# Kernel tuning notes

Measured on AMD Instinct MI355X. Metric: run time of the kernel, lower is better.

Reference implementation:

```python
import jax, jax.numpy as jnp
import numpy as np

N_NODES = 100000
N_EDGES = 625000
D = 128
DEPTH = 2
BN_EPS = 1e-5


def setup_inputs() -> dict:
    key = jax.random.key(0)
    ks = jax.random.split(key, 8)
    x = jax.random.normal(ks[0], (N_NODES, D), dtype=jnp.float32)
    edge_index = jax.random.randint(ks[1], (2, N_EDGES), 0, N_NODES, dtype=jnp.int64)
    edge_weight = jax.random.uniform(ks[2], (N_EDGES,), dtype=jnp.float32)
    s = 1.0 / np.sqrt(D)
    W_lin = jax.random.uniform(ks[3], (DEPTH, D, D), jnp.float32, -s, s)
    W_gcn = jax.random.uniform(ks[4], (DEPTH, D, D), jnp.float32, -s, s)
    gamma = jnp.ones((DEPTH, D), jnp.float32)
    beta = jnp.zeros((DEPTH, D), jnp.float32)
    return {"x": x, "edge_index": edge_index, "edge_weight": edge_weight,
            "W_lin": W_lin, "W_gcn": W_gcn, "gamma": gamma, "beta": beta}


def reference(x, edge_index, edge_weight, W_lin, W_gcn, gamma, beta):
    n = x.shape[0]
    row, col = edge_index[0], edge_index[1]  # source, target
    # gcn_norm with add_self_loops=False: deg over targets, symmetric normalization
    deg = jax.ops.segment_sum(edge_weight, col, num_segments=n)
    dinv = jnp.where(deg > 0, jax.lax.rsqrt(deg), 0.0)
    norm = dinv[row] * edge_weight * dinv[col]  # [E]

    for i in range(DEPTH):
        hl = x @ W_lin[i].T                       # parallel linear branch
        hg = x @ W_gcn[i].T                       # GCNConv linear
        msg = norm[:, None] * hg[row]             # [E, D] messages
        hr = jax.ops.segment_sum(msg, col, num_segments=n)
        h = hl + hr
        # BatchNorm1d, training mode (batch statistics, biased variance)
        mu = jnp.mean(h, axis=0)
        var = jnp.mean((h - mu) ** 2, axis=0)
        h = (h - mu) * jax.lax.rsqrt(var + BN_EPS) * gamma[i] + beta[i]
        x = jnp.maximum(h, 0.0) if i != DEPTH - 1 else h
    return x
```

## Files before the change

### kernel.cpp

```cpp
#include <hip/hip_runtime.h>

#define NN 100000
#define NE 625000
#define DD 128
#define CAP 32
#define NREP 8

#define CONVB 12500
#define WPACKB 256
#define FILL2B ((NE / 2 + 255) / 256)
#define GB ((NN + 63) / 64)

typedef __attribute__((ext_vector_type(8))) short bf16x8;
typedef __attribute__((ext_vector_type(4))) float f32x4;

static __device__ __forceinline__ unsigned short f2bf(float f) {
    union { float f; unsigned u; } v; v.f = f;
    unsigned u = v.u + 0x7fffu + ((v.u >> 16) & 1u);
    return (unsigned short)(u >> 16);
}
static __device__ __forceinline__ float bflo(unsigned u) { return __uint_as_float(u << 16); }
static __device__ __forceinline__ float bfhi(unsigned u) { return __uint_as_float(u & 0xffff0000u); }

static __device__ __forceinline__ void foldLDS(const float* __restrict__ stats,
                                               const float* __restrict__ gamma,
                                               const float* __restrict__ beta,
                                               float* sSc, float* sSh, int t) {
    if (t < 128) {
        float sum = 0.f, sq = 0.f;
        #pragma unroll
        for (int rp = 0; rp < NREP; rp++) {
            sum += stats[rp * 256 + t];
            sq  += stats[rp * 256 + 128 + t];
        }
        float mu = sum * (1.0f / NN);
        float var = sq * (1.0f / NN) - mu * mu;
        float is = rsqrtf(var + 1e-5f);
        float sc = is * gamma[t];
        sSc[t] = sc;
        sSh[t] = beta[t] - mu * sc;
    }
}

__global__ __launch_bounds__(256) void k_fill(const int* __restrict__ row,
                                              const int* __restrict__ col,
                                              const float* __restrict__ w,
                                              int* __restrict__ cnt,
                                              int2* __restrict__ ebuf) {
    int id = blockIdx.x * 256 + threadIdx.x;
    if (id < NE / 2) {
        int e = id * 2;
        int2 rr = *(const int2*)&row[e];
        int2 cc = *(const int2*)&col[e];
        float2 ww = *(const float2*)&w[e];
        int p0 = atomicAdd(&cnt[cc.x], 1);
        int p1 = atomicAdd(&cnt[cc.y], 1);
        if (p0 < CAP) {
            int2 v; v.x = rr.x; v.y = __float_as_int(ww.x);
            ebuf[(size_t)cc.x * CAP + p0] = v;
        }
        if (p1 < CAP) {
            int2 v; v.x = rr.y; v.y = __float_as_int(ww.y);
            ebuf[(size_t)cc.y * CAP + p1] = v;
        }
    }
}

__global__ __launch_bounds__(256) void k_conv(const float* __restrict__ x,
                                              unsigned* __restrict__ Xb2,
                                              const float* __restrict__ Wl,
                                              const float* __restrict__ Wg,
                                              unsigned short* __restrict__ wp) {
    int b = blockIdx.x, t = threadIdx.x;
    if (b < WPACKB) {
        int idx = b * 256 + t;
        int l = idx >> 15;
        int rem = idx & 32767;
        int n = rem >> 8;
        int k = rem & 255;
        float v = (k < 128) ? Wl[(size_t)l * DD * DD + n * DD + k]
                            : Wg[(size_t)l * DD * DD + n * DD + (k - 128)];
        int wv = n >> 5;
        int tt = (n >> 4) & 1;
        int i  = n & 15;
        int ss = k >> 5;
        int q  = (k >> 3) & 3;
        int j  = k & 7;
        size_t off = ((size_t)((((l * 4 + wv) * 2 + tt) * 8 + ss)) * 64 + q * 16 + i) * 8 + j;
        wp[off] = f2bf(v);
    } else {
        size_t i = (size_t)(b - WPACKB) * 256 + t;
        size_t base = i * 4;
        float4 v = *(const float4*)&x[base];
        uint2 o;
        o.x = (unsigned)f2bf(v.x) | ((unsigned)f2bf(v.y) << 16);
        o.y = (unsigned)f2bf(v.z) | ((unsigned)f2bf(v.w) << 16);
        *(uint2*)&Xb2[i * 2] = o;
    }
}

__global__ __launch_bounds__(256) void k_dinvb(const int* __restrict__ cnt,
                                               const int2* __restrict__ ebuf,
                                               float* __restrict__ dinv) {
    int t = threadIdx.x;
    int node = blockIdx.x * 32 + (t >> 3);
    int l = t & 7;
    int c = cnt[node]; if (c > CAP) c = CAP;
    float s = 0.f;
    for (int p = l; p < c; p += 8) s += __int_as_float(ebuf[(size_t)node * CAP + p].y);
    s += __shfl_down(s, 4, 8);
    s += __shfl_down(s, 2, 8);
    s += __shfl_down(s, 1, 8);
    if (l == 0) dinv[node] = (s > 0.f) ? rsqrtf(s) : 0.f;
}

template<int LAYER>
__global__ __launch_bounds__(256) void k_gatherP(const int* __restrict__ cnt,
                                                 const int2* __restrict__ ebuf,
                                                 const float* __restrict__ dinv,
                                                 const unsigned* __restrict__ X2,
                                                 const float* __restrict__ stats,
                                                 const float* __restrict__ gamma,
                                                 const float* __restrict__ beta,
                                                 unsigned* __restrict__ P2) {
    __shared__ float sSc[128], sSh[128];
    const int t = threadIdx.x;
    const int wave = t >> 6;
    const int lane = t & 63;
    float scx = 0.f, scy = 0.f, shx = 0.f, shy = 0.f;
    if (LAYER) {
        foldLDS(stats, gamma, beta, sSc, sSh, t);
        __syncthreads();
        scx = sSc[2 * lane]; scy = sSc[2 * lane + 1];
        shx = sSh[2 * lane]; shy = sSh[2 * lane + 1];
    }

    const int node0 = blockIdx.x * 8 + wave * 2;
    const int node1 = node0 + 1;
    int c0 = cnt[node0]; if (c0 > CAP) c0 = CAP;
    int c1 = cnt[node1]; if (c1 > CAP) c1 = CAP;
    const int2* eb0 = ebuf + (size_t)node0 * CAP;
    const int2* eb1 = ebuf + (size_t)node1 * CAP;
    float ax0 = 0.f, ay0 = 0.f, ax1 = 0.f, ay1 = 0.f;

    auto chunk4 = [&](const int2* __restrict__ eb, int p, float& ax, float& ay) {
        int2 e0 = eb[p], e1 = eb[p + 1], e2 = eb[p + 2], e3 = eb[p + 3];
        float w0 = __int_as_float(e0.y) * dinv[e0.x];
        float w1 = __int_as_float(e1.y) * dinv[e1.x];
        float w2 = __int_as_float(e2.y) * dinv[e2.x];
        float w3 = __int_as_float(e3.y) * dinv[e3.x];
        unsigned u0 = X2[(size_t)e0.x * 64 + lane];
        unsigned u1 = X2[(size_t)e1.x * 64 + lane];
        unsigned u2 = X2[(size_t)e2.x * 64 + lane];
        unsigned u3 = X2[(size_t)e3.x * 64 + lane];
        float x0 = bflo(u0), y0 = bfhi(u0);
        float x1 = bflo(u1), y1 = bfhi(u1);
        float x2 = bflo(u2), y2 = bfhi(u2);
        float x3 = bflo(u3), y3 = bfhi(u3);
        if (LAYER) {
            x0 = fmaxf(x0 * scx + shx, 0.f); y0 = fmaxf(y0 * scy + shy, 0.f);
            x1 = fmaxf(x1 * scx + shx, 0.f); y1 = fmaxf(y1 * scy + shy, 0.f);
            x2 = fmaxf(x2 * scx + shx, 0.f); y2 = fmaxf(y2 * scy + shy, 0.f);
            x3 = fmaxf(x3 * scx + shx, 0.f); y3 = fmaxf(y3 * scy + shy, 0.f);
        }
        ax += w0 * x0 + w1 * x1 + w2 * x2 + w3 * x3;
        ay += w0 * y0 + w1 * y1 + w2 * y2 + w3 * y3;
    };
    auto edge1 = [&](const int2* __restrict__ eb, int p, float& ax, float& ay) {
        int2 e0 = eb[p];
        float w0 = __int_as_float(e0.y) * dinv[e0.x];
        unsigned u0 = X2[(size_t)e0.x * 64 + lane];
        float x0 = bflo(u0), y0 = bfhi(u0);
        if (LAYER) {
            x0 = fmaxf(x0 * scx + shx, 0.f); y0 = fmaxf(y0 * scy + shy, 0.f);
        }
        ax += w0 * x0;
        ay += w0 * y0;
    };

    const int mc = (c0 < c1) ? c0 : c1;
    int p = 0;
    for (; p + 3 < mc; p += 4) {
        chunk4(eb0, p, ax0, ay0);
        chunk4(eb1, p, ax1, ay1);
    }
    int p0 = p, p1 = p;
    for (; p0 + 3 < c0; p0 += 4) chunk4(eb0, p0, ax0, ay0);
    for (; p0 < c0; p0++)        edge1(eb0, p0, ax0, ay0);
    for (; p1 + 3 < c1; p1 += 4) chunk4(eb1, p1, ax1, ay1);
    for (; p1 < c1; p1++)        edge1(eb1, p1, ax1, ay1);

    float dn0 = dinv[node0], dn1 = dinv[node1];
    ax0 *= dn0; ay0 *= dn0;
    ax1 *= dn1; ay1 *= dn1;
    P2[(size_t)node0 * 64 + lane] = (unsigned)f2bf(ax0) | ((unsigned)f2bf(ay0) << 16);
    P2[(size_t)node1 * 64 + lane] = (unsigned)f2bf(ax1) | ((unsigned)f2bf(ay1) << 16);
}

template<int LAYER>
__global__ __launch_bounds__(256, 5) void k_gemm_s(const unsigned short* Xin,
                                                   const unsigned short* P,
                                                   const unsigned short* __restrict__ wp,
                                                   const float* __restrict__ statsIn,
                                                   const float* __restrict__ gammaIn,
                                                   const float* __restrict__ betaIn,
                                                   unsigned short* Hout,
                                                   float* __restrict__ statsOut) {
    __shared__ __align__(16) char smem[22528];
    unsigned short* sA = (unsigned short*)smem;
    float* red2 = (float*)(smem + 17408);
    float* sSc = (float*)(smem + 21504);
    float* sSh = (float*)(smem + 22016);

    const int t = threadIdx.x;
    const int wave = t >> 6;
    const int lane = t & 63;
    const int i16 = lane & 15;
    const int quad = lane >> 4;
    const int rowBase = blockIdx.x * 64;

    if (LAYER == 1) {
        foldLDS(statsIn, gammaIn, betaIn, sSc, sSh, t);
        __syncthreads();
    }

    f32x4 acc[4][2] = {{{0.f,0.f,0.f,0.f}}};

    #pragma unroll
    for (int rep = 0; rep < 4; rep++) {
        int lin = rep * 2048 + t * 8;
        int r = lin >> 7, c = lin & 127;
        int rr = rowBase + r; if (rr >= NN) rr = NN - 1;
        uint4 u = *(const uint4*)&Xin[(size_t)rr * DD + c];
        if (LAYER == 1) {
            float4 sc0 = *(const float4*)&sSc[c];
            float4 sc1 = *(const float4*)&sSc[c + 4];
            float4 sh0 = *(const float4*)&sSh[c];
            float4 sh1 = *(const float4*)&sSh[c + 4];
            float v0 = fmaxf(bflo(u.x) * sc0.x + sh0.x, 0.f);
            float v1 = fmaxf(bfhi(u.x) * sc0.y + sh0.y, 0.f);
            float v2 = fmaxf(bflo(u.y) * sc0.z + sh0.z, 0.f);
            float v3 = fmaxf(bfhi(u.y) * sc0.w + sh0.w, 0.f);
            float v4 = fmaxf(bflo(u.z) * sc1.x + sh1.x, 0.f);
            float v5 = fmaxf(bfhi(u.z) * sc1.y + sh1.y, 0.f);
            float v6 = fmaxf(bflo(u.w) * sc1.z + sh1.z, 0.f);
            float v7 = fmaxf(bfhi(u.w) * sc1.w + sh1.w, 0.f);
            u.x = (unsigned)f2bf(v0) | ((unsigned)f2bf(v1) << 16);
            u.y = (unsigned)f2bf(v2) | ((unsigned)f2bf(v3) << 16);
            u.z = (unsigned)f2bf(v4) | ((unsigned)f2bf(v5) << 16);
            u.w = (unsigned)f2bf(v6) | ((unsigned)f2bf(v7) << 16);
        }
        *(uint4*)&sA[r * 136 + c] = u;
    }
    __syncthreads();
    {
        bf16x8 wf[2][4];
        #pragma unroll
        for (int tt = 0; tt < 2; tt++)
            #pragma unroll
            for (int ss = 0; ss < 4; ss++) {
                size_t off = ((size_t)(((wave * 2 + tt) * 8 + ss)) * 64 + quad * 16 + i16) * 8;
                wf[tt][ss] = *(const bf16x8*)&wp[off];
            }
        #pragma unroll
        for (int ss = 0; ss < 4; ss++) {
            bf16x8 af[4];
            #pragma unroll
            for (int mt = 0; mt < 4; mt++)
                af[mt] = *(const bf16x8*)&sA[(mt * 16 + i16) * 136 + ss * 32 + quad * 8];
            #pragma unroll
            for (int mt = 0; mt < 4; mt++)
                #pragma unroll
                for (int tt = 0; tt < 2; tt++)
                    acc[mt][tt] = __builtin_amdgcn_mfma_f32_16x16x32_bf16(
                        af[mt], wf[tt][ss], acc[mt][tt], 0, 0, 0);
        }
    }
    __syncthreads();

    #pragma unroll
    for (int rep = 0; rep < 4; rep++) {
        int lin = rep * 2048 + t * 8;
        int r = lin >> 7, c = lin & 127;
        int rr = rowBase + r; if (rr >= NN) rr = NN - 1;
        uint4 u = *(const uint4*)&P[(size_t)rr * DD + c];
        *(uint4*)&sA[r * 136 + c] = u;
    }
    __syncthreads();
    {
        bf16x8 wf[2][4];
        #pragma unroll
        for (int tt = 0; tt < 2; tt++)
            #pragma unroll
            for (int ss = 0; ss < 4; ss++) {
                size_t off = ((size_t)(((wave * 2 + tt) * 8 + ss + 4)) * 64 + quad * 16 + i16) * 8;
                wf[tt][ss] = *(const bf16x8*)&wp[off];
            }
        #pragma unroll
        for (int ss = 0; ss < 4; ss++) {
            bf16x8 af[4];
            #pragma unroll
            for (int mt = 0; mt < 4; mt++)
                af[mt] = *(const bf16x8*)&sA[(mt * 16 + i16) * 136 + ss * 32 + quad * 8];
            #pragma unroll
            for (int mt = 0; mt < 4; mt++)
                #pragma unroll
                for (int tt = 0; tt < 2; tt++)
                    acc[mt][tt] = __builtin_amdgcn_mfma_f32_16x16x32_bf16(
                        af[mt], wf[tt][ss], acc[mt][tt], 0, 0, 0);
        }
    }
    __syncthreads();

    #pragma unroll
    for (int mt = 0; mt < 4; mt++)
        #pragma unroll
        for (int r = 0; r < 4; r++) {
            int row = mt * 16 + quad * 4 + r;
            #pragma unroll
            for (int tt = 0; tt < 2; tt++)
                sA[row * 136 + wave * 32 + tt * 16 + i16] = f2bf(acc[mt][tt][r]);
        }
    __syncthreads();

    float s[8] = {0.f,0.f,0.f,0.f,0.f,0.f,0.f,0.f};
    float q[8] = {0.f,0.f,0.f,0.f,0.f,0.f,0.f,0.f};
    const int cg = t & 15;
    #pragma unroll
    for (int it = 0; it < 4; it++) {
        int row = it * 16 + (t >> 4);
        int gr = rowBase + row;
        uint4 v = *(const uint4*)&sA[row * 136 + cg * 8];
        float m = (gr < NN) ? 1.f : 0.f;
        if (gr < NN) *(uint4*)&Hout[(size_t)gr * DD + cg * 8] = v;
        float e0 = bflo(v.x) * m, e1 = bfhi(v.x) * m;
        float e2 = bflo(v.y) * m, e3 = bfhi(v.y) * m;
        float e4 = bflo(v.z) * m, e5 = bfhi(v.z) * m;
        float e6 = bflo(v.w) * m, e7 = bfhi(v.w) * m;
        s[0] += e0; q[0] += e0 * e0;  s[1] += e1; q[1] += e1 * e1;
        s[2] += e2; q[2] += e2 * e2;  s[3] += e3; q[3] += e3 * e3;
        s[4] += e4; q[4] += e4 * e4;  s[5] += e5; q[5] += e5 * e5;
        s[6] += e6; q[6] += e6 * e6;  s[7] += e7; q[7] += e7 * e7;
    }
    #pragma unroll
    for (int j = 0; j < 8; j++) {
        s[j] += __shfl_xor(s[j], 16);
        s[j] += __shfl_xor(s[j], 32);
        q[j] += __shfl_xor(q[j], 16);
        q[j] += __shfl_xor(q[j], 32);
    }
    if (lane < 16) {
        #pragma unroll
        for (int j = 0; j < 8; j++) {
            red2[(wave * 16 + lane) * 16 + j]     = s[j];
            red2[(wave * 16 + lane) * 16 + 8 + j] = q[j];
        }
    }
    __syncthreads();
    {
        int colx = t & 127;
        int type = t >> 7;
        int j = type * 8 + (colx & 7);
        int cgx = colx >> 3;
        float tot = red2[(0 * 16 + cgx) * 16 + j] + red2[(1 * 16 + cgx) * 16 + j]
                  + red2[(2 * 16 + cgx) * 16 + j] + red2[(3 * 16 + cgx) * 16 + j];
        atomicAdd(&statsOut[(blockIdx.x & (NREP - 1)) * 256 + type * 128 + colx], tot);
    }
}

__global__ __launch_bounds__(256) void k_apply_out(const unsigned* __restrict__ H2,
                                                   const float* __restrict__ stats,
                                                   const float* __restrict__ gamma,
                                                   const float* __restrict__ beta,
                                                   float* __restrict__ out) {
    __shared__ __align__(16) float sSc[128];
    __shared__ __align__(16) float sSh[128];
    int t = threadIdx.x;
    foldLDS(stats, gamma, beta, sSc, sSh, t);
    __syncthreads();
    size_t i = (size_t)blockIdx.x * 256 + t;
    size_t base = i * 4;
    int c = (int)(base & 127);
    uint2 u = *(const uint2*)&H2[i * 2];
    float4 sc = *(const float4*)&sSc[c];
    float4 sh = *(const float4*)&sSh[c];
    float4 o;
    o.x = bflo(u.x) * sc.x + sh.x;
    o.y = bfhi(u.x) * sc.y + sh.y;
    o.z = bflo(u.y) * sc.z + sh.z;
    o.w = bfhi(u.y) * sc.w + sh.w;
    *(float4*)&out[base] = o;
}

extern "C" void kernel_launch(void* const* d_in, const int* in_sizes, int n_in,
                              void* d_out, int out_size, void* d_ws, size_t ws_size,
                              hipStream_t stream) {
    const float* x_in  = (const float*)d_in[0];
    const int*   ei    = (const int*)d_in[1];
    const float* ew    = (const float*)d_in[2];
    const float* Wl    = (const float*)d_in[3];
    const float* Wg    = (const float*)d_in[4];
    const float* gamma = (const float*)d_in[5];
    const float* beta  = (const float*)d_in[6];
    float* out = (float*)d_out;

    char* p = (char*)d_ws;
    unsigned short* bufA = (unsigned short*)p; p += (size_t)NN * DD * 2;
    unsigned short* bufB = (unsigned short*)p; p += (size_t)NN * DD * 2;
    int2* ebuf  = (int2*)p;  p += (size_t)NN * CAP * 8;
    int*   cnt    = (int*)p;   p += (size_t)NN * 4;
    float* stats0 = (float*)p; p += NREP * 256 * 4;
    float* stats1 = (float*)p; p += NREP * 256 * 4;
    float* dinv   = (float*)p; p += 400000;
    unsigned short* wpack = (unsigned short*)p; p += 65536 * 2;

    const int* row = ei;
    const int* col = ei + NE;

    hipMemsetAsync(cnt, 0, (size_t)NN * 4 + 2 * NREP * 256 * 4, stream);
    k_fill<<<FILL2B, 256, 0, stream>>>(row, col, ew, cnt, ebuf);
    k_conv<<<WPACKB + CONVB, 256, 0, stream>>>(x_in, (unsigned*)bufA, Wl, Wg, wpack);
    k_dinvb<<<NN / 32, 256, 0, stream>>>(cnt, ebuf, dinv);

    k_gatherP<0><<<NN / 8, 256, 0, stream>>>(cnt, ebuf, dinv, (const unsigned*)bufA,
                                             nullptr, nullptr, nullptr, (unsigned*)bufB);
    k_gemm_s<0><<<GB, 256, 0, stream>>>(bufA, bufB, wpack,
                                        nullptr, nullptr, nullptr, bufA, stats0);

    k_gatherP<1><<<NN / 8, 256, 0, stream>>>(cnt, ebuf, dinv, (const unsigned*)bufA,
                                             stats0, gamma, beta, (unsigned*)bufB);
    k_gemm_s<1><<<GB, 256, 0, stream>>>(bufA, bufB, wpack + 32768,
                                        stats0, gamma, beta, bufB, stats1);

    k_apply_out<<<NN * DD / 1024, 256, 0, stream>>>((const unsigned*)bufB, stats1,
                                                    gamma + DD, beta + DD, out);
}
```

Before: 291.8 us.

## Build compact CSR edge buffer via count, scan, and fill passes

Replaces the fixed-capacity per-node padded edge slots (NN*CAP) with a compact CSR layout built by counting in-degrees, taking a block-level prefix scan with an atomic global base, then filling edges at scanned offsets. The counting is fused into the conversion kernel launch. The compact buffer is meant to shrink the edge footprint and improve locality of edge reads in the gather and degree kernels. In exchange it adds two extra kernel launches, a second pass of atomics over the columns, and an offsets lookup per node. Node ranges are not globally ordered across blocks because the base offset comes from an atomic.

Result: slower. 333.8 us (+14.4%).

```diff
diff --git a/kernel.cpp b/kernel.cpp
--- a/kernel.cpp
+++ b/kernel.cpp
@@ -8,7 +8,9 @@
 
 #define CONVB 12500
 #define WPACKB 256
+#define COUNTB ((NE / 4) / 256 + 1)
 #define FILL2B ((NE / 2 + 255) / 256)
+#define SCANB ((NN + 255) / 256)
 #define GB ((NN + 63) / 64)
 
 typedef __attribute__((ext_vector_type(8))) short bf16x8;
@@ -42,38 +44,25 @@
     }
 }
 
-__global__ __launch_bounds__(256) void k_fill(const int* __restrict__ row,
-                                              const int* __restrict__ col,
-                                              const float* __restrict__ w,
-                                              int* __restrict__ cnt,
-                                              int2* __restrict__ ebuf) {
-    int id = blockIdx.x * 256 + threadIdx.x;
-    if (id < NE / 2) {
-        int e = id * 2;
-        int2 rr = *(const int2*)&row[e];
-        int2 cc = *(const int2*)&col[e];
-        float2 ww = *(const float2*)&w[e];
-        int p0 = atomicAdd(&cnt[cc.x], 1);
-        int p1 = atomicAdd(&cnt[cc.y], 1);
-        if (p0 < CAP) {
-            int2 v; v.x = rr.x; v.y = __float_as_int(ww.x);
-            ebuf[(size_t)cc.x * CAP + p0] = v;
-        }
-        if (p1 < CAP) {
-            int2 v; v.x = rr.y; v.y = __float_as_int(ww.y);
-            ebuf[(size_t)cc.y * CAP + p1] = v;
-        }
-    }
-}
-
-__global__ __launch_bounds__(256) void k_conv(const float* __restrict__ x,
-                                              unsigned* __restrict__ Xb2,
-                                              const float* __restrict__ Wl,
-                                              const float* __restrict__ Wg,
-                                              unsigned short* __restrict__ wp) {
+__global__ __launch_bounds__(256) void k_cc(const float* __restrict__ x,
+                                            unsigned* __restrict__ Xb2,
+                                            const float* __restrict__ Wl,
+                                            const float* __restrict__ Wg,
+                                            unsigned short* __restrict__ wp,
+                                            const int* __restrict__ col,
+                                            int* __restrict__ cnt) {
     int b = blockIdx.x, t = threadIdx.x;
-    if (b < WPACKB) {
-        int idx = b * 256 + t;
+    if (b < COUNTB) {
+        int id = b * 256 + t;
+        if (id < NE / 4) {
+            int4 cc = *(const int4*)&col[id * 4];
+            atomicAdd(&cnt[cc.x], 1);
+            atomicAdd(&cnt[cc.y], 1);
+            atomicAdd(&cnt[cc.z], 1);
+            atomicAdd(&cnt[cc.w], 1);
+        }
+    } else if (b < COUNTB + WPACKB) {
+        int idx = (b - COUNTB) * 256 + t;
         int l = idx >> 15;
         int rem = idx & 32767;
         int n = rem >> 8;
@@ -89,7 +78,7 @@
         size_t off = ((size_t)((((l * 4 + wv) * 2 + tt) * 8 + ss)) * 64 + q * 16 + i) * 8 + j;
         wp[off] = f2bf(v);
     } else {
-        size_t i = (size_t)(b - WPACKB) * 256 + t;
+        size_t i = (size_t)(b - COUNTB - WPACKB) * 256 + t;
         size_t base = i * 4;
         float4 v = *(const float4*)&x[base];
         uint2 o;
@@ -99,15 +88,69 @@
     }
 }
 
+__global__ __launch_bounds__(256) void k_scan(const int* __restrict__ cnt,
+                                              int* __restrict__ offs,
+                                              int* __restrict__ cur,
+                                              int* __restrict__ gcur) {
+    __shared__ int ls[256];
+    __shared__ int lbase;
+    int t = threadIdx.x;
+    int node = blockIdx.x * 256 + t;
+    int c = 0;
+    if (node < NN) { c = cnt[node]; if (c > CAP) c = CAP; }
+    ls[t] = c;
+    __syncthreads();
+    for (int d = 1; d < 256; d <<= 1) {
+        int add = (t >= d) ? ls[t - d] : 0;
+        __syncthreads();
+        ls[t] += add;
+        __syncthreads();
+    }
+    if (t == 255) lbase = atomicAdd(gcur, ls[255]);
+    __syncthreads();
+    if (node < NN) {
+        int o = lbase + ls[t] - c;
+        offs[node] = o;
+        cur[node]  = o;
+    }
+}
+
+__global__ __launch_bounds__(256) void k_fill2(const int* __restrict__ row,
+                                               const int* __restrict__ col,
+                                               const float* __restrict__ w,
+                                               const int* __restrict__ offs,
+                                               int* __restrict__ cur,
+                                               int2* __restrict__ ebufC) {
+    int id = blockIdx.x * 256 + threadIdx.x;
+    if (id < NE / 2) {
+        int e = id * 2;
+        int2 rr = *(const int2*)&row[e];
+        int2 cc = *(const int2*)&col[e];
+        float2 ww = *(const float2*)&w[e];
+        int p0 = atomicAdd(&cur[cc.x], 1);
+        int p1 = atomicAdd(&cur[cc.y], 1);
+        if (p0 - offs[cc.x] < CAP) {
+            int2 v; v.x = rr.x; v.y = __float_as_int(ww.x);
+            ebufC[p0] = v;
+        }
+        if (p1 - offs[cc.y] < CAP) {
+            int2 v; v.x = rr.y; v.y = __float_as_int(ww.y);
+            ebufC[p1] = v;
+        }
+    }
+}
+
 __global__ __launch_bounds__(256) void k_dinvb(const int* __restrict__ cnt,
-                                               const int2* __restrict__ ebuf,
+                                               const int* __restrict__ offs,
+                                               const int2* __restrict__ ebufC,
                                                float* __restrict__ dinv) {
     int t = threadIdx.x;
     int node = blockIdx.x * 32 + (t >> 3);
     int l = t & 7;
     int c = cnt[node]; if (c > CAP) c = CAP;
+    const int2* eb = ebufC + offs[node];
     float s = 0.f;
-    for (int p = l; p < c; p += 8) s += __int_as_float(ebuf[(size_t)node * CAP + p].y);
+    for (int p = l; p < c; p += 8) s += __int_as_float(eb[p].y);
     s += __shfl_down(s, 4, 8);
     s += __shfl_down(s, 2, 8);
     s += __shfl_down(s, 1, 8);
@@ -116,7 +159,8 @@
 
 template<int LAYER>
 __global__ __launch_bounds__(256) void k_gatherP(const int* __restrict__ cnt,
-                                                 const int2* __restrict__ ebuf,
+                                                 const int* __restrict__ offs,
+                                                 const int2* __restrict__ ebufC,
                                                  const float* __restrict__ dinv,
                                                  const unsigned* __restrict__ X2,
                                                  const float* __restrict__ stats,
@@ -139,8 +183,8 @@
     const int node1 = node0 + 1;
     int c0 = cnt[node0]; if (c0 > CAP) c0 = CAP;
     int c1 = cnt[node1]; if (c1 > CAP) c1 = CAP;
-    const int2* eb0 = ebuf + (size_t)node0 * CAP;
-    const int2* eb1 = ebuf + (size_t)node1 * CAP;
+    const int2* eb0 = ebufC + offs[node0];
+    const int2* eb1 = ebufC + offs[node1];
     float ax0 = 0.f, ay0 = 0.f, ax1 = 0.f, ay1 = 0.f;
 
     auto chunk4 = [&](const int2* __restrict__ eb, int p, float& ax, float& ay) {
@@ -407,27 +451,32 @@
     char* p = (char*)d_ws;
     unsigned short* bufA = (unsigned short*)p; p += (size_t)NN * DD * 2;
     unsigned short* bufB = (unsigned short*)p; p += (size_t)NN * DD * 2;
-    int2* ebuf  = (int2*)p;  p += (size_t)NN * CAP * 8;
+    int2* ebufC = (int2*)p;  p += (size_t)NE * 8;
     int*   cnt    = (int*)p;   p += (size_t)NN * 4;
+    int*   gcur   = (int*)p;   p += 64;
     float* stats0 = (float*)p; p += NREP * 256 * 4;
     float* stats1 = (float*)p; p += NREP * 256 * 4;
+    int*   offs   = (int*)p;   p += (size_t)NN * 4;
+    int*   cur    = (int*)p;   p += (size_t)NN * 4;
     float* dinv   = (float*)p; p += 400000;
     unsigned short* wpack = (unsigned short*)p; p += 65536 * 2;
 
     const int* row = ei;
     const int* col = ei + NE;
 
-    hipMemsetAsync(cnt, 0, (size_t)NN * 4 + 2 * NREP * 256 * 4, stream);
-    k_fill<<<FILL2B, 256, 0, stream>>>(row, col, ew, cnt, ebuf);
-    k_conv<<<WPACKB + CONVB, 256, 0, stream>>>(x_in, (unsigned*)bufA, Wl, Wg, wpack);
-    k_dinvb<<<NN / 32, 256, 0, stream>>>(cnt, ebuf, dinv);
-
-    k_gatherP<0><<<NN / 8, 256, 0, stream>>>(cnt, ebuf, dinv, (const unsigned*)bufA,
+    hipMemsetAsync(cnt, 0, (size_t)NN * 4 + 64 + 2 * NREP * 256 * 4, stream);
+    k_cc<<<COUNTB + WPACKB + CONVB, 256, 0, stream>>>(
+        x_in, (unsigned*)bufA, Wl, Wg, wpack, col, cnt);
+    k_scan<<<SCANB, 256, 0, stream>>>(cnt, offs, cur, gcur);
+    k_fill2<<<FILL2B, 256, 0, stream>>>(row, col, ew, offs, cur, ebufC);
+    k_dinvb<<<NN / 32, 256, 0, stream>>>(cnt, offs, ebufC, dinv);
+
+    k_gatherP<0><<<NN / 8, 256, 0, stream>>>(cnt, offs, ebufC, dinv, (const unsigned*)bufA,
                                              nullptr, nullptr, nullptr, (unsigned*)bufB);
     k_gemm_s<0><<<GB, 256, 0, stream>>>(bufA, bufB, wpack,
                                         nullptr, nullptr, nullptr, bufA, stats0);
 
-    k_gatherP<1><<<NN / 8, 256, 0, stream>>>(cnt, ebuf, dinv, (const unsigned*)bufA,
+    k_gatherP<1><<<NN / 8, 256, 0, stream>>>(cnt, offs, ebufC, dinv, (const unsigned*)bufA,
                                              stats0, gamma, beta, (unsigned*)bufB);
     k_gemm_s<1><<<GB, 256, 0, stream>>>(bufA, bufB, wpack + 32768,
                                         stats0, gamma, beta, bufB, stats1);
```
